# Optimization experiments

Measured on AMD Instinct MI355X. Metric: run time of the kernel, lower is better.

## Reference

```python
import jax, jax.numpy as jnp
import numpy as np

# Model/config constants (match init_kwargs)
B, S, D, H = 2, 2048, 512, 8
HD = D // H            # head dim = 64
WIN, DIL, G = 16, 2, 64  # window size, dilation rate, num global tokens
L = S - G              # 1984 local tokens (global indices are 0..G-1)


def setup_inputs() -> dict:
    key = jax.random.key(0)
    ks = jax.random.split(key, 16)
    sc = 0.02
    n = jax.random.normal
    return {
        "query": n(ks[0], (B, S, D), jnp.float32),
        "key": n(ks[1], (B, S, D), jnp.float32),
        "value": n(ks[2], (B, S, D), jnp.float32),
        # local multi-head attention params (linear_query/key/value/out_proj)
        "wq": n(ks[3], (D, D), jnp.float32) * sc, "bq": jnp.zeros((D,), jnp.float32),
        "wk": n(ks[4], (D, D), jnp.float32) * sc, "bk": jnp.zeros((D,), jnp.float32),
        "wv": n(ks[5], (D, D), jnp.float32) * sc, "bv": jnp.zeros((D,), jnp.float32),
        "wo": n(ks[6], (D, D), jnp.float32) * sc, "bo": jnp.zeros((D,), jnp.float32),
        # global nn.MultiheadAttention params (packed in_proj + out_proj)
        "g_in_w": n(ks[7], (3 * D, D), jnp.float32) * sc,
        "g_in_b": jnp.zeros((3 * D,), jnp.float32),
        "g_out_w": n(ks[8], (D, D), jnp.float32) * sc,
        "g_out_b": jnp.zeros((D,), jnp.float32),
    }


def _window_indices():
    # centered dilated window per local position, clipped to valid range
    pos = jnp.arange(L)
    offs = DIL * (jnp.arange(WIN) - WIN // 2)
    return jnp.clip(pos[:, None] + offs[None, :], 0, L - 1)


def reference(query, key, value, wq, bq, wk, bk, wv, bv, wo, bo,
              g_in_w, g_in_b, g_out_w, g_out_b):
    scale = 1.0 / np.sqrt(HD).astype(np.float32)

    # ---- local (dilated sliding window) path over tokens G..S-1 ----
    q_loc = query[:, G:, :]                      # (B, L, D)
    widx = _window_indices()
    k_win = key[:, G:, :][:, widx, :]
    v_win = value[:, G:, :][:, widx, :]

    q = (q_loc @ wq.T + bq).reshape(B, L, H, HD)          # (B,L,H,HD)
    k = (k_win @ wk.T + bk).reshape(B, L, WIN, H, HD)     # (B,L,W,H,HD)
    v = (v_win @ wv.T + bv).reshape(B, L, WIN, H, HD)

    scores = jnp.einsum('blhd,blwhd->blhw', q, k) * scale
    p = jax.nn.softmax(scores, axis=-1)
    o = jnp.einsum('blhw,blwhd->blhd', p, v).reshape(B, L, D)
    local_out = o @ wo.T + bo                              # (B,L,D)

    # ---- global token path: standard MHA over the G global tokens ----
    wq_g, wk_g, wv_g = g_in_w[:D], g_in_w[D:2 * D], g_in_w[2 * D:]
    bq_g, bk_g, bv_g = g_in_b[:D], g_in_b[D:2 * D], g_in_b[2 * D:]
    qg = (query[:, :G] @ wq_g.T + bq_g).reshape(B, G, H, HD)
    kg = (key[:, :G] @ wk_g.T + bk_g).reshape(B, G, H, HD)
    vg = (value[:, :G] @ wv_g.T + bv_g).reshape(B, G, H, HD)
    sg = jnp.einsum('bqhd,bkhd->bhqk', qg, kg) * scale     # (B,H,G,G)
    pg = jax.nn.softmax(sg, axis=-1)
    og = jnp.einsum('bhqk,bkhd->bqhd', pg, vg).reshape(B, G, D)
    global_out = og @ g_out_w.T + g_out_b                  # (B,G,D)

    # ---- fuse: scatter local + global back into full sequence ----
    out = jnp.zeros((B, S, D), query.dtype)
    out = out.at[:, G:, :].set(local_out)
    out = out.at[:, :G, :].set(global_out)
    return out
```

## Files before the change

kernel.cpp:

```cpp
#include <hip/hip_runtime.h>
#include <stdint.h>

#define B_ 2
#define S_ 2048
#define D_ 512
#define H_ 8
#define WIN_ 16
#define DIL_ 2
#define G_ 64
#define L_ (S_ - G_)

typedef short bf16x8 __attribute__((ext_vector_type(8)));
typedef float f32x4 __attribute__((ext_vector_type(4)));
typedef unsigned short u16;

#define LDSW 36

__device__ __forceinline__ float bf2f(u16 h) {
  return __uint_as_float(((uint32_t)h) << 16);
}
__device__ __forceinline__ u16 f2bf(float f) {
  uint32_t u = __float_as_uint(f);
  uint32_t r = (u + 0x7fffu + ((u >> 16) & 1u)) >> 16;
  return (u16)r;
}
__device__ __forceinline__ uint32_t pack2(float lo, float hi) {
  return (uint32_t)f2bf(lo) | ((uint32_t)f2bf(hi) << 16);
}

struct Job {
  const void* X; const float* W; const float* bias; void* Y;
  int rpb;
  int xoff;
  long xbs;
  int yoff;
  long ybs;
  int out_f32;
};
struct GemmLaunch { int start[6]; Job job[6]; };

template <int X_BF16>
__global__ __launch_bounds__(256) void gemm_kernel(GemmLaunch a) {
  int bid = (int)blockIdx.x;
  bid = (bid & 7) * ((int)gridDim.x >> 3) + (bid >> 3);

  int j = 0;
#pragma unroll
  for (int i = 1; i < 6; ++i) j = (bid >= a.start[i]) ? i : j;
  const Job jb = a.job[j];
  bid -= a.start[j];
  const int tm = bid >> 3, tn = bid & 7;
  const int row0 = tm * 128, n0 = tn * 64;

  __shared__ __align__(16) u16 As[2][128 * LDSW];
  __shared__ __align__(16) u16 Bs[2][64 * LDSW];

  const int tid = threadIdx.x, lane = tid & 63, w = tid >> 6;
  const int wm = w >> 1, wn = w & 1;

  const int rs = tid >> 2;
  const int kq = (tid & 3) * 8;

  const int r0 = row0 + rs,      b0 = r0 >= jb.rpb;
  const int r1 = row0 + 64 + rs, b1 = r1 >= jb.rpb;
  const size_t xi0 = (size_t)(b0 ? jb.xbs : 0) +
                     (size_t)(jb.xoff + r0 - (b0 ? jb.rpb : 0)) * 512 + kq;
  const size_t xi1 = (size_t)(b1 ? jb.xbs : 0) +
                     (size_t)(jb.xoff + r1 - (b1 ? jb.rpb : 0)) * 512 + kq;
  const float* wb0 = jb.W + (size_t)(n0 + rs) * 512 + kq;

  f32x4 acc[4][2];
#pragma unroll
  for (int i = 0; i < 4; ++i)
#pragma unroll
    for (int k = 0; k < 2; ++k) acc[i][k] = (f32x4){0.f, 0.f, 0.f, 0.f};

  auto cvt_store_f32 = [&](const float* src, u16* dst) {
    float4 lo = *(const float4*)src;
    float4 hi = *(const float4*)(src + 4);
    int4 p;
    p.x = (int)pack2(lo.x, lo.y);
    p.y = (int)pack2(lo.z, lo.w);
    p.z = (int)pack2(hi.x, hi.y);
    p.w = (int)pack2(hi.z, hi.w);
    *(int4*)dst = p;
  };
  auto stage = [&](int buf, int kof) {
    if (X_BF16) {
      const u16* xb = (const u16*)jb.X;
      *(int4*)&As[buf][rs * LDSW + kq]        = *(const int4*)&xb[xi0 + kof];
      *(int4*)&As[buf][(64 + rs) * LDSW + kq] = *(const int4*)&xb[xi1 + kof];
    } else {
      const float* xf = (const float*)jb.X;
      cvt_store_f32(xf + xi0 + kof, &As[buf][rs * LDSW + kq]);
      cvt_store_f32(xf + xi1 + kof, &As[buf][(64 + rs) * LDSW + kq]);
    }
    cvt_store_f32(wb0 + kof, &Bs[buf][rs * LDSW + kq]);
  };
  auto compute = [&](int buf) {
    bf16x8 af[4], bfv[2];
#pragma unroll
    for (int fm = 0; fm < 4; ++fm)
      af[fm] = *(const bf16x8*)&As[buf][(wm * 64 + fm * 16 + (lane & 15)) * LDSW + 8 * (lane >> 4)];
#pragma unroll
    for (int fn = 0; fn < 2; ++fn)
      bfv[fn] = *(const bf16x8*)&Bs[buf][(wn * 32 + fn * 16 + (lane & 15)) * LDSW + 8 * (lane >> 4)];
#pragma unroll
    for (int fm = 0; fm < 4; ++fm)
#pragma unroll
      for (int fn = 0; fn < 2; ++fn)
        acc[fm][fn] = __builtin_amdgcn_mfma_f32_16x16x32_bf16(af[fm], bfv[fn], acc[fm][fn], 0, 0, 0);
  };

  stage(0, 0);
  __syncthreads();
  int cur = 0;
  for (int kt = 0; kt < 15; ++kt) {
    stage(cur ^ 1, (kt + 1) * 32);
    compute(cur);
    __syncthreads();
    cur ^= 1;
  }
  compute(cur);

#pragma unroll
  for (int fm = 0; fm < 4; ++fm) {
#pragma unroll
    for (int fn = 0; fn < 2; ++fn) {
#pragma unroll
      for (int r = 0; r < 4; ++r) {
        const int row = row0 + wm * 64 + fm * 16 + (lane >> 4) * 4 + r;
        const int col = n0 + wn * 32 + fn * 16 + (lane & 15);
        const int b = row >= jb.rpb;
        const int rr = row - (b ? jb.rpb : 0);
        const size_t yi = (size_t)(b ? jb.ybs : 0) + (size_t)(jb.yoff + rr) * 512 + col;
        const float v = acc[fm][fn][r] + jb.bias[col];
        if (jb.out_f32) ((float*)jb.Y)[yi] = v;
        else            ((u16*)jb.Y)[yi]   = f2bf(v);
      }
    }
  }
}

__global__ __launch_bounds__(256) void attn_kernel(const u16* qp, const u16* kp,
                                                   const u16* vp, u16* ob,
                                                   const u16* qgp, const u16* kgp,
                                                   const u16* vgp, u16* ogp) {
  const int lane = threadIdx.x & 63;
  int bid = (int)blockIdx.x;
  const int nbl = (B_ * L_) / 4;
  if (bid < nbl) bid = (bid & 7) * (nbl >> 3) + (bid >> 3);
  const int wid = bid * 4 + (threadIdx.x >> 6);

  if (wid < B_ * L_) {
    const int l = wid % L_;
    const int brow = wid - l;
    float q[8];
    {
      bf16x8 qv = *(const bf16x8*)&qp[(size_t)wid * 512 + lane * 8];
#pragma unroll
      for (int e = 0; e < 8; ++e) q[e] = bf2f((u16)qv[e]);
    }
    float s[WIN_];
#pragma unroll
    for (int w2 = 0; w2 < WIN_; ++w2) {
      int ki = l + DIL_ * w2 - WIN_;
      ki = ki < 0 ? 0 : (ki > L_ - 1 ? L_ - 1 : ki);
      bf16x8 kv = *(const bf16x8*)&kp[(size_t)(brow + ki) * 512 + lane * 8];
      float p = 0.f;
#pragma unroll
      for (int e = 0; e < 8; ++e) p = fmaf(q[e], bf2f((u16)kv[e]), p);
      p += __shfl_xor(p, 1); p += __shfl_xor(p, 2); p += __shfl_xor(p, 4);
      s[w2] = p * 0.125f;
    }
    float m = s[0];
#pragma unroll
    for (int w2 = 1; w2 < WIN_; ++w2) m = fmaxf(m, s[w2]);
    float sum = 0.f;
#pragma unroll
    for (int w2 = 0; w2 < WIN_; ++w2) { s[w2] = __expf(s[w2] - m); sum += s[w2]; }
    const float inv = 1.0f / sum;
    float acc[8] = {0.f};
#pragma unroll
    for (int w2 = 0; w2 < WIN_; ++w2) {
      int ki = l + DIL_ * w2 - WIN_;
      ki = ki < 0 ? 0 : (ki > L_ - 1 ? L_ - 1 : ki);
      bf16x8 vv = *(const bf16x8*)&vp[(size_t)(brow + ki) * 512 + lane * 8];
#pragma unroll
      for (int e = 0; e < 8; ++e) acc[e] = fmaf(s[w2], bf2f((u16)vv[e]), acc[e]);
    }
    bf16x8 o8;
#pragma unroll
    for (int e = 0; e < 8; ++e) o8[e] = (short)f2bf(acc[e] * inv);
    *(bf16x8*)&ob[(size_t)wid * 512 + lane * 8] = o8;
  } else {
    const int g = wid - B_ * L_;
    const int base = (g >> 6) * 64;
    const int qi = g & 63;
    float q[8];
    {
      bf16x8 qv = *(const bf16x8*)&qgp[(size_t)(base + qi) * 512 + lane * 8];
#pragma unroll
      for (int e = 0; e < 8; ++e) q[e] = bf2f((u16)qv[e]);
    }
    float m = -1e30f, sum = 0.f, acc[8] = {0.f};
    for (int j2 = 0; j2 < 64; ++j2) {
      bf16x8 kv = *(const bf16x8*)&kgp[(size_t)(base + j2) * 512 + lane * 8];
      float p = 0.f;
#pragma unroll
      for (int e = 0; e < 8; ++e) p = fmaf(q[e], bf2f((u16)kv[e]), p);
      p += __shfl_xor(p, 1); p += __shfl_xor(p, 2); p += __shfl_xor(p, 4);
      p *= 0.125f;
      const float mn = fmaxf(m, p);
      const float c  = __expf(m - mn);
      const float pe = __expf(p - mn);
      sum = sum * c + pe;
      m = mn;
      bf16x8 vv = *(const bf16x8*)&vgp[(size_t)(base + j2) * 512 + lane * 8];
#pragma unroll
      for (int e = 0; e < 8; ++e) acc[e] = acc[e] * c + pe * bf2f((u16)vv[e]);
    }
    const float inv = 1.0f / sum;
    bf16x8 o8;
#pragma unroll
    for (int e = 0; e < 8; ++e) o8[e] = (short)f2bf(acc[e] * inv);
    *(bf16x8*)&ogp[(size_t)(base + qi) * 512 + lane * 8] = o8;
  }
}

extern "C" void kernel_launch(void* const* d_in, const int* in_sizes, int n_in,
                              void* d_out, int out_size, void* d_ws, size_t ws_size,
                              hipStream_t stream) {
  const float* query   = (const float*)d_in[0];
  const float* key     = (const float*)d_in[1];
  const float* value   = (const float*)d_in[2];
  const float* wq      = (const float*)d_in[3];
  const float* bq      = (const float*)d_in[4];
  const float* wk      = (const float*)d_in[5];
  const float* bk      = (const float*)d_in[6];
  const float* wv      = (const float*)d_in[7];
  const float* bv      = (const float*)d_in[8];
  const float* wo      = (const float*)d_in[9];
  const float* bo      = (const float*)d_in[10];
  const float* g_in_w  = (const float*)d_in[11];
  const float* g_in_b  = (const float*)d_in[12];
  const float* g_out_w = (const float*)d_in[13];
  const float* g_out_b = (const float*)d_in[14];
  float* out = (float*)d_out;

  u16* w16 = (u16*)d_ws;
  const size_t PSZ = (size_t)B_ * L_ * D_;
  const size_t GSZ = (size_t)B_ * G_ * D_;

  u16* qp  = w16;        u16* kp  = qp + PSZ;   u16* vp  = kp + PSZ;
  u16* ob  = vp + PSZ;
  u16* qgp = ob + PSZ;   u16* kgp = qgp + GSZ;  u16* vgp = kgp + GSZ;
  u16* ogp = vgp + GSZ;

  const long XBS = (long)S_ * D_;
  const long PBS = (long)L_ * D_;
  const long GBS = (long)G_ * D_;

  GemmLaunch gi;
  gi.start[0] = 0; gi.start[1] = 248; gi.start[2] = 496;
  gi.start[3] = 744; gi.start[4] = 752; gi.start[5] = 760;
  gi.job[0] = {query, wq, bq, qp, L_, G_, XBS, 0, PBS, 0};
  gi.job[1] = {key,   wk, bk, kp, L_, G_, XBS, 0, PBS, 0};
  gi.job[2] = {value, wv, bv, vp, L_, G_, XBS, 0, PBS, 0};
  gi.job[3] = {query, g_in_w,             g_in_b,          qgp, G_, 0, XBS, 0, GBS, 0};
  gi.job[4] = {key,   g_in_w + 512 * D_,  g_in_b + D_,     kgp, G_, 0, XBS, 0, GBS, 0};
  gi.job[5] = {value, g_in_w + 1024 * D_, g_in_b + 2 * D_, vgp, G_, 0, XBS, 0, GBS, 0};
  hipLaunchKernelGGL(gemm_kernel<0>, dim3(768), dim3(256), 0, stream, gi);

  hipLaunchKernelGGL(attn_kernel, dim3((B_ * L_ + 128) / 4), dim3(256), 0, stream,
                     qp, kp, vp, ob, qgp, kgp, vgp, ogp);

  GemmLaunch go;
  go.start[0] = 0; go.start[1] = 248;
  go.start[2] = go.start[3] = go.start[4] = go.start[5] = 0x7fffffff;
  go.job[0] = {ob,  wo,      bo,      out, L_, 0, PBS, G_, XBS, 1};
  go.job[1] = {ogp, g_out_w, g_out_b, out, G_, 0, GBS, 0,  XBS, 1};
  go.job[2] = go.job[1]; go.job[3] = go.job[1]; go.job[4] = go.job[1]; go.job[5] = go.job[1];
  hipLaunchKernelGGL(gemm_kernel<1>, dim3(256), dim3(256), 0, stream, go);
}
```

Before: 182.5 us.

## Prefetch GEMM tiles into registers two stages ahead and pad LDS rows

Restructures the projection GEMM main loop so global loads for the next K-tile are issued into registers before the current tile's MFMA compute, with conversion and LDS writes deferred until after compute. The aim is to hide global-load latency behind MFMA work instead of stalling on loads inside the staging step. LDS row stride also changes from 36 to 40 to alter the bank-conflict pattern. The cost is higher register pressure from two sets of staging registers, which could lower occupancy.

Measured after the change: 162.2 us. 1.13x faster.

```diff
diff --git a/kernel.cpp b/kernel.cpp
--- a/kernel.cpp
+++ b/kernel.cpp
@@ -14,7 +14,7 @@
 typedef float f32x4 __attribute__((ext_vector_type(4)));
 typedef unsigned short u16;
 
-#define LDSW 36
+#define LDSW 40
 
 __device__ __forceinline__ float bf2f(u16 h) {
   return __uint_as_float(((uint32_t)h) << 16);
@@ -75,27 +75,75 @@
 #pragma unroll
     for (int k = 0; k < 2; ++k) acc[i][k] = (f32x4){0.f, 0.f, 0.f, 0.f};
 
-  auto cvt_store_f32 = [&](const float* src, u16* dst) {
-    float4 lo = *(const float4*)src;
-    float4 hi = *(const float4*)(src + 4);
-    int4 p;
-    p.x = (int)pack2(lo.x, lo.y);
-    p.y = (int)pack2(lo.z, lo.w);
-    p.z = (int)pack2(hi.x, hi.y);
-    p.w = (int)pack2(hi.z, hi.w);
-    *(int4*)dst = p;
-  };
-  auto stage = [&](int buf, int kof) {
-    if (X_BF16) {
+  f32x4 Aa0, Aa1, Aa2, Aa3, Aw0, Aw1;
+  f32x4 Ba0, Ba1, Ba2, Ba3, Bw0, Bw1;
+  int4  Ax0, Ax1, Bx0, Bx1;
+
+  auto issueA = [&](int kof) {
+    if constexpr (X_BF16) {
       const u16* xb = (const u16*)jb.X;
-      *(int4*)&As[buf][rs * LDSW + kq]        = *(const int4*)&xb[xi0 + kof];
-      *(int4*)&As[buf][(64 + rs) * LDSW + kq] = *(const int4*)&xb[xi1 + kof];
+      Ax0 = *(const int4*)&xb[xi0 + kof];
+      Ax1 = *(const int4*)&xb[xi1 + kof];
     } else {
       const float* xf = (const float*)jb.X;
-      cvt_store_f32(xf + xi0 + kof, &As[buf][rs * LDSW + kq]);
-      cvt_store_f32(xf + xi1 + kof, &As[buf][(64 + rs) * LDSW + kq]);
-    }
-    cvt_store_f32(wb0 + kof, &Bs[buf][rs * LDSW + kq]);
+      Aa0 = *(const f32x4*)(xf + xi0 + kof);
+      Aa1 = *(const f32x4*)(xf + xi0 + kof + 4);
+      Aa2 = *(const f32x4*)(xf + xi1 + kof);
+      Aa3 = *(const f32x4*)(xf + xi1 + kof + 4);
+    }
+    Aw0 = *(const f32x4*)(wb0 + kof);
+    Aw1 = *(const f32x4*)(wb0 + kof + 4);
+  };
+  auto issueB = [&](int kof) {
+    if constexpr (X_BF16) {
+      const u16* xb = (const u16*)jb.X;
+      Bx0 = *(const int4*)&xb[xi0 + kof];
+      Bx1 = *(const int4*)&xb[xi1 + kof];
+    } else {
+      const float* xf = (const float*)jb.X;
+      Ba0 = *(const f32x4*)(xf + xi0 + kof);
+      Ba1 = *(const f32x4*)(xf + xi0 + kof + 4);
+      Ba2 = *(const f32x4*)(xf + xi1 + kof);
+      Ba3 = *(const f32x4*)(xf + xi1 + kof + 4);
+    }
+    Bw0 = *(const f32x4*)(wb0 + kof);
+    Bw1 = *(const f32x4*)(wb0 + kof + 4);
+  };
+  auto writeA = [&](int buf) {
+    if constexpr (X_BF16) {
+      *(int4*)&As[buf][rs * LDSW + kq]        = Ax0;
+      *(int4*)&As[buf][(64 + rs) * LDSW + kq] = Ax1;
+    } else {
+      int4 p;
+      p.x = (int)pack2(Aa0[0], Aa0[1]); p.y = (int)pack2(Aa0[2], Aa0[3]);
+      p.z = (int)pack2(Aa1[0], Aa1[1]); p.w = (int)pack2(Aa1[2], Aa1[3]);
+      *(int4*)&As[buf][rs * LDSW + kq] = p;
+      p.x = (int)pack2(Aa2[0], Aa2[1]); p.y = (int)pack2(Aa2[2], Aa2[3]);
+      p.z = (int)pack2(Aa3[0], Aa3[1]); p.w = (int)pack2(Aa3[2], Aa3[3]);
+      *(int4*)&As[buf][(64 + rs) * LDSW + kq] = p;
+    }
+    int4 pw;
+    pw.x = (int)pack2(Aw0[0], Aw0[1]); pw.y = (int)pack2(Aw0[2], Aw0[3]);
+    pw.z = (int)pack2(Aw1[0], Aw1[1]); pw.w = (int)pack2(Aw1[2], Aw1[3]);
+    *(int4*)&Bs[buf][rs * LDSW + kq] = pw;
+  };
+  auto writeB = [&](int buf) {
+    if constexpr (X_BF16) {
+      *(int4*)&As[buf][rs * LDSW + kq]        = Bx0;
+      *(int4*)&As[buf][(64 + rs) * LDSW + kq] = Bx1;
+    } else {
+      int4 p;
+      p.x = (int)pack2(Ba0[0], Ba0[1]); p.y = (int)pack2(Ba0[2], Ba0[3]);
+      p.z = (int)pack2(Ba1[0], Ba1[1]); p.w = (int)pack2(Ba1[2], Ba1[3]);
+      *(int4*)&As[buf][rs * LDSW + kq] = p;
+      p.x = (int)pack2(Ba2[0], Ba2[1]); p.y = (int)pack2(Ba2[2], Ba2[3]);
+      p.z = (int)pack2(Ba3[0], Ba3[1]); p.w = (int)pack2(Ba3[2], Ba3[3]);
+      *(int4*)&As[buf][(64 + rs) * LDSW + kq] = p;
+    }
+    int4 pw;
+    pw.x = (int)pack2(Bw0[0], Bw0[1]); pw.y = (int)pack2(Bw0[2], Bw0[3]);
+    pw.z = (int)pack2(Bw1[0], Bw1[1]); pw.w = (int)pack2(Bw1[2], Bw1[3]);
+    *(int4*)&Bs[buf][rs * LDSW + kq] = pw;
   };
   auto compute = [&](int buf) {
     bf16x8 af[4], bfv[2];
@@ -112,16 +160,24 @@
         acc[fm][fn] = __builtin_amdgcn_mfma_f32_16x16x32_bf16(af[fm], bfv[fn], acc[fm][fn], 0, 0, 0);
   };
 
-  stage(0, 0);
+  issueA(0);
+  issueB(32);
+  writeA(0);
   __syncthreads();
-  int cur = 0;
-  for (int kt = 0; kt < 15; ++kt) {
-    stage(cur ^ 1, (kt + 1) * 32);
-    compute(cur);
+  for (int t = 0; t < 14; t += 2) {
+    issueA((t + 2) * 32);
+    compute(0);
+    writeB(1);
     __syncthreads();
-    cur ^= 1;
+    issueB((t + 3) * 32);
+    compute(1);
+    writeA(0);
+    __syncthreads();
   }
-  compute(cur);
+  compute(0);
+  writeB(1);
+  __syncthreads();
+  compute(1);
 
 #pragma unroll
   for (int fm = 0; fm < 4; ++fm) {
```
